# Performance work log

Hardware: AMD Instinct MI355X
Metric: run time of the kernel (lower is better)

## Reference

```python
import jax, jax.numpy as jnp
import numpy as np

B, T, E, H = 2, 4096, 768, 12
D = E // H  # head_dim = 64


def setup_inputs() -> dict:
    key = jax.random.key(0)
    ks = jax.random.split(key, 9)
    s = 1.0 / np.sqrt(E)
    return {
        "x": jax.random.normal(ks[0], (B, T, E), dtype=jnp.float32),
        "wq": jax.random.normal(ks[1], (E, E), dtype=jnp.float32) * s,
        "bq": jnp.zeros((E,), dtype=jnp.float32),
        "wk": jax.random.normal(ks[2], (E, E), dtype=jnp.float32) * s,
        "bk": jnp.zeros((E,), dtype=jnp.float32),
        "wv": jax.random.normal(ks[3], (E, E), dtype=jnp.float32) * s,
        "bv": jnp.zeros((E,), dtype=jnp.float32),
        "wo": jax.random.normal(ks[4], (E, E), dtype=jnp.float32) * s,
        "bo": jnp.zeros((E,), dtype=jnp.float32),
    }


def reference(x, wq, bq, wk, bk, wv, bv, wo, bo):
    # Linear projections (torch Linear: x @ W.T + b; weights here stored as (in,out))
    q = x @ wq + bq  # (B,T,E)
    k = x @ wk + bk
    v = x @ wv + bv

    def split(t):
        return t.reshape(B, T, H, D).transpose(0, 2, 1, 3)  # (B,H,T,D)

    q, k, v = split(q), split(k), split(v)
    scale = 1.0 / np.sqrt(D).astype(np.float32)
    scores = jnp.einsum("bhtd,bhsd->bhts", q, k) * scale  # (B,H,T,T)
    causal = jnp.tril(jnp.ones((T, T), dtype=bool))
    scores = jnp.where(causal, scores, -jnp.inf)
    attn = jax.nn.softmax(scores, axis=-1)
    out = jnp.einsum("bhts,bhsd->bhtd", attn, v)  # (B,H,T,D)
    out = out.transpose(0, 2, 1, 3).reshape(B, T, E)
    return out @ wo + bo
```

## Files before the change

### kernel.cpp

```cpp
#include <hip/hip_runtime.h>
#include <hip/hip_bf16.h>

#define TSEQ 4096
#define EMB 768
#define NH 12
#define DH 64
#define BT 8192

typedef __attribute__((ext_vector_type(8))) short bf16x8;
typedef __attribute__((ext_vector_type(4))) float f32x4;

#define FENCE() asm volatile("" ::: "memory")

__device__ __forceinline__ f32x4 mfma16(bf16x8 a, bf16x8 b, f32x4 c) {
    return __builtin_amdgcn_mfma_f32_16x16x32_bf16(a, b, c, 0, 0, 0);
}

__device__ __forceinline__ void gload16(const void* g, void* l) {
    __builtin_amdgcn_global_load_lds((const __attribute__((address_space(1))) void*)g,
                                     (__attribute__((address_space(3))) void*)l, 16, 0, 0);
}

__global__ __launch_bounds__(256) void conv_x_k(const float* __restrict__ x,
                                                __hip_bfloat16* __restrict__ xb) {
    int i = (blockIdx.x * 256 + threadIdx.x) * 4;
    float4 v = *(const float4*)(x + i);
    union { unsigned short u[4]; uint2 p; } o;
    __hip_bfloat16 t0 = __float2bfloat16(v.x); o.u[0] = *(unsigned short*)&t0;
    __hip_bfloat16 t1 = __float2bfloat16(v.y); o.u[1] = *(unsigned short*)&t1;
    __hip_bfloat16 t2 = __float2bfloat16(v.z); o.u[2] = *(unsigned short*)&t2;
    __hip_bfloat16 t3 = __float2bfloat16(v.w); o.u[3] = *(unsigned short*)&t3;
    *(uint2*)(xb + i) = o.p;
}

__global__ __launch_bounds__(256) void conv_w_k(const float* w0, const float* w1,
                                                const float* w2, const float* w3,
                                                __hip_bfloat16* o0, __hip_bfloat16* o1,
                                                __hip_bfloat16* o2, __hip_bfloat16* o3) {
    const float* w; __hip_bfloat16* o;
    switch (blockIdx.z) {
        case 0: w = w0; o = o0; break;
        case 1: w = w1; o = o1; break;
        case 2: w = w2; o = o2; break;
        default: w = w3; o = o3; break;
    }
    __shared__ float tile[32][33];
    int tx = threadIdx.x & 31, ty = threadIdx.x >> 5;
    int kb = blockIdx.y * 32, nb = blockIdx.x * 32;
    for (int i = 0; i < 32; i += 8)
        tile[ty + i][tx] = w[(size_t)(kb + ty + i) * EMB + nb + tx];
    __syncthreads();
    for (int i = 0; i < 32; i += 8)
        o[(size_t)(nb + ty + i) * EMB + kb + tx] = __float2bfloat16(tile[tx][ty + i]);
}

__device__ __forceinline__ void gemm_body(const __hip_bfloat16* __restrict__ A,
                                          const __hip_bfloat16* __restrict__ Wt,
                                          const float* __restrict__ bias,
                                          void* __restrict__ outp, int mode, float scale) {
    __shared__ alignas(16) char As[2][8192];
    __shared__ alignas(16) char Bs[2][8192];
    const int m0 = blockIdx.x * 128, n0 = blockIdx.y * 128;
    const int tid = threadIdx.x;
    const int lane = tid & 63, l15 = lane & 15, lg = lane >> 4;
    const int wave = tid >> 6, wm = wave >> 1, wn = wave & 1;
    const int swz = (l15 & 7) << 4;

    int mrow_[2]; int kelem_[2];
#pragma unroll
    for (int c = 0; c < 2; ++c) {
        int p = c * 4096 + tid * 16;
        int lrow = p >> 7, w = p & 127;
        int wp = w ^ ((lrow & 7) << 4);
        mrow_[c] = lrow + ((wp >> 6) & 1) * 64;
        kelem_[c] = (wp & 63) >> 1;
    }

    f32x4 acc[4][4];
    for (int i = 0; i < 4; ++i)
        for (int j = 0; j < 4; ++j) acc[i][j] = (f32x4){0.f, 0.f, 0.f, 0.f};

    auto stage = [&](int buf, int k0) {
#pragma unroll
        for (int c = 0; c < 2; ++c)
            gload16(A + (size_t)(m0 + mrow_[c]) * EMB + k0 + kelem_[c],
                    As[buf] + c * 4096 + wave * 1024);
#pragma unroll
        for (int c = 0; c < 2; ++c)
            gload16(Wt + (size_t)(n0 + mrow_[c]) * EMB + k0 + kelem_[c],
                    Bs[buf] + c * 4096 + wave * 1024);
    };

    stage(0, 0);
    const int NK = EMB / 32;
    for (int ks = 0; ks < NK; ++ks) {
        const int cur = ks & 1;
        const bool pre = (ks + 1 < NK);
        if (pre) stage(cur ^ 1, (ks + 1) * 32);
        if (pre) asm volatile("s_waitcnt vmcnt(4)" ::: "memory");
        else     asm volatile("s_waitcnt vmcnt(0)" ::: "memory");
        FENCE(); __builtin_amdgcn_s_barrier(); FENCE();
        bf16x8 af[4], bfv[4];
#pragma unroll
        for (int f = 0; f < 4; ++f)
            af[f] = *(const bf16x8*)(As[cur] + (f * 16 + l15) * 128 + ((wm * 64 + lg * 16) ^ swz));
#pragma unroll
        for (int f = 0; f < 4; ++f)
            bfv[f] = *(const bf16x8*)(Bs[cur] + (f * 16 + l15) * 128 + ((wn * 64 + lg * 16) ^ swz));
        __builtin_amdgcn_s_setprio(1);
#pragma unroll
        for (int i = 0; i < 4; ++i)
#pragma unroll
            for (int j = 0; j < 4; ++j)
                acc[i][j] = mfma16(af[i], bfv[j], acc[i][j]);
        __builtin_amdgcn_s_setprio(0);
        FENCE(); __builtin_amdgcn_s_barrier(); FENCE();
    }

#pragma unroll
    for (int i = 0; i < 4; ++i) {
#pragma unroll
        for (int j = 0; j < 4; ++j) {
            const int n = n0 + wn * 64 + j * 16 + l15;
            const float bv = bias[n];
            const int mbase = m0 + wm * 64 + i * 16 + lg * 4;
#pragma unroll
            for (int r = 0; r < 4; ++r) {
                const int m = mbase + r;
                const float val = (acc[i][j][r] + bv) * scale;
                if (mode == 2) {
                    ((float*)outp)[(size_t)m * EMB + n] = val;
                } else {
                    const int b = m >> 12, t = m & (TSEQ - 1);
                    const int h = n >> 6, d = n & 63;
                    size_t addr;
                    if (mode == 0) addr = ((size_t)(b * NH + h) * TSEQ + t) * DH + d;
                    else           addr = ((size_t)(b * NH + h) * DH + d) * TSEQ + t;
                    ((__hip_bfloat16*)outp)[addr] = __float2bfloat16(val);
                }
            }
        }
    }
}

__global__ __launch_bounds__(256) void qkv_k(const __hip_bfloat16* __restrict__ xb,
                                             const __hip_bfloat16* __restrict__ wqT,
                                             const __hip_bfloat16* __restrict__ wkT,
                                             const __hip_bfloat16* __restrict__ wvT,
                                             const float* __restrict__ bq,
                                             const float* __restrict__ bk,
                                             const float* __restrict__ bv,
                                             __hip_bfloat16* __restrict__ qo,
                                             __hip_bfloat16* __restrict__ ko,
                                             __hip_bfloat16* __restrict__ vo) {
    const __hip_bfloat16* Wt; const float* bias; void* o; int mode; float scale;
    const float cq = 0.125f * 1.44269504089f;
    switch (blockIdx.z) {
        case 0:  Wt = wqT; bias = bq; o = qo; mode = 0; scale = cq;  break;
        case 1:  Wt = wkT; bias = bk; o = ko; mode = 0; scale = 1.f; break;
        default: Wt = wvT; bias = bv; o = vo; mode = 1; scale = 1.f; break;
    }
    gemm_body(xb, Wt, bias, o, mode, scale);
}

__global__ __launch_bounds__(256) void oproj_k(const __hip_bfloat16* __restrict__ abf,
                                               const __hip_bfloat16* __restrict__ woT,
                                               const float* __restrict__ bo,
                                               float* __restrict__ out) {
    gemm_body(abf, woT, bo, out, 2, 1.f);
}

__global__ __launch_bounds__(256, 3) void attn_k(const __hip_bfloat16* __restrict__ qb,
                                                 const __hip_bfloat16* __restrict__ kb,
                                                 const __hip_bfloat16* __restrict__ vt,
                                                 __hip_bfloat16* __restrict__ ab) {
    __shared__ alignas(16) char Ks[2][8192];
    __shared__ alignas(16) char Vs[2][8192];
    __shared__ alignas(16) char pbuf[4][4096];
    const int lane = threadIdx.x & 63, l15 = lane & 15, lg = lane >> 4;
    const int wave = threadIdx.x >> 6;
    const int bid = blockIdx.x;
    const int xcd = bid & 7, slot = bid >> 3;
    const int pair = slot & 31, hgrp = slot >> 5;
    const int bh = xcd + hgrp * 8;
    const __hip_bfloat16* Qh = qb + (size_t)bh * TSEQ * DH;
    const __hip_bfloat16* Kh = kb + (size_t)bh * TSEQ * DH;
    const __hip_bfloat16* Vh = vt + (size_t)bh * DH * TSEQ;
    char* Pb = pbuf[wave];
    const int swz = (l15 & 7) << 4;
    const int b = bh / NH, h = bh % NH;
    const float M0 = 12.0f;

    bf16x8 ones8;
#pragma unroll
    for (int j = 0; j < 8; ++j) ones8[j] = (short)0x3F80;

    unsigned ka[8];
#pragma unroll
    for (int st = 0; st < 4; ++st)
#pragma unroll
        for (int ks = 0; ks < 2; ++ks)
            ka[st * 2 + ks] = (unsigned)((st * 16 + l15) * 128 + ((ks * 64 + lg * 16) ^ swz));
    char* pwh[4]; char* prh[2]; char* pwl[4]; char* prl[2];
#pragma unroll
    for (int st = 0; st < 4; ++st) {
        pwh[st] = Pb + l15 * 128 + ((st * 32 + lg * 8) ^ swz);
        pwl[st] = pwh[st] + 2048;
    }
#pragma unroll
    for (int ks = 0; ks < 2; ++ks) {
        prh[ks] = Pb + l15 * 128 + ((ks * 64 + lg * 16) ^ swz);
        prl[ks] = prh[ks] + 2048;
    }
    const int dthr = wave * 16 + l15 - lg * 4;

    int r_[2], wp_[2];
#pragma unroll
    for (int c = 0; c < 2; ++c) {
        int p = c * 4096 + wave * 1024 + lane * 16;
        int r = p >> 7, w = p & 127;
        r_[c] = r;
        wp_[c] = (w ^ ((r & 7) << 4)) >> 1;
    }

    const int lo = pair, hi = 63 - pair;
    const int q0l = lo * 64 + wave * 16;
    const int q0h = hi * 64 + wave * 16;
    const int nsb = hi + 1;

    bf16x8 qh0 = *(const bf16x8*)(Qh + (size_t)(q0h + l15) * DH + lg * 8);
    bf16x8 qh1 = *(const bf16x8*)(Qh + (size_t)(q0h + l15) * DH + 32 + lg * 8);
    bf16x8 ql0 = *(const bf16x8*)(Qh + (size_t)(q0l + l15) * DH + lg * 8);
    bf16x8 ql1 = *(const bf16x8*)(Qh + (size_t)(q0l + l15) * DH + 32 + lg * 8);

    f32x4 oh[4], ol[4];
#pragma unroll
    for (int dt = 0; dt < 4; ++dt) { oh[dt] = (f32x4){0.f,0.f,0.f,0.f}; ol[dt] = (f32x4){0.f,0.f,0.f,0.f}; }
    f32x4 lh = (f32x4){0.f,0.f,0.f,0.f}, ll = (f32x4){0.f,0.f,0.f,0.f};

    const char* kg0 = (const char*)(Kh + (size_t)r_[0] * DH + wp_[0]);
    const char* kg1 = (const char*)(Kh + (size_t)r_[1] * DH + wp_[1]);
    const char* vg0 = (const char*)(Vh + (size_t)r_[0] * TSEQ + wp_[0]);
    const char* vg1 = (const char*)(Vh + (size_t)r_[1] * TSEQ + wp_[1]);

#define STAGE(DST) do {                                                          \
    gload16(kg0, Ks[DST] + wave * 1024);                                         \
    gload16(kg1, Ks[DST] + 4096 + wave * 1024);                                  \
    gload16(vg0, Vs[DST] + wave * 1024);                                         \
    gload16(vg1, Vs[DST] + 4096 + wave * 1024);                                  \
    kg0 += 8192; kg1 += 8192; vg0 += 128; vg1 += 128;                            \
} while (0)

#define QKSM(KF, Q0, Q1, MASKB, PW) do {                                         \
    f32x4 sa[4];                                                                 \
    __builtin_amdgcn_s_setprio(1);                                               \
    _Pragma("unroll")                                                            \
    for (int st = 0; st < 4; ++st) {                                             \
        f32x4 z = (f32x4){0.f, 0.f, 0.f, 0.f};                                   \
        z = mfma16(KF[st * 2 + 0], Q0, z);                                       \
        z = mfma16(KF[st * 2 + 1], Q1, z);                                       \
        sa[st] = z;                                                              \
    }                                                                            \
    __builtin_amdgcn_s_setprio(0);                                               \
    if (MASKB) {                                                                 \
        _Pragma("unroll")                                                        \
        for (int st = 0; st < 4; ++st)                                           \
            _Pragma("unroll")                                                    \
            for (int r = 0; r < 4; ++r)                                          \
                if (st * 16 + r > dthr) sa[st][r] = -INFINITY;                   \
    }                                                                            \
    _Pragma("unroll")                                                            \
    for (int st = 0; st < 4; ++st) {                                             \
        const float e0 = exp2f(sa[st][0] - M0);                                  \
        const float e1 = exp2f(sa[st][1] - M0);                                  \
        const float e2 = exp2f(sa[st][2] - M0);                                  \
        const float e3 = exp2f(sa[st][3] - M0);                                  \
        uint2 pkv;                                                               \
        asm("v_cvt_pk_bf16_f32 %0, %1, %2" : "=v"(pkv.x) : "v"(e0), "v"(e1));    \
        asm("v_cvt_pk_bf16_f32 %0, %1, %2" : "=v"(pkv.y) : "v"(e2), "v"(e3));    \
        *(uint2*)PW[st] = pkv;                                                   \
    }                                                                            \
} while (0)

#define PVU(VF, OV, LA, PR) do {                                                 \
    bf16x8 pf0 = *(const bf16x8*)PR[0];                                          \
    bf16x8 pf1 = *(const bf16x8*)PR[1];                                          \
    __builtin_amdgcn_s_setprio(1);                                               \
    LA = mfma16(pf0, ones8, LA);                                                 \
    LA = mfma16(pf1, ones8, LA);                                                 \
    _Pragma("unroll")                                                            \
    for (int dt = 0; dt < 4; ++dt)                                               \
        OV[dt] = mfma16(pf0, VF[dt * 2 + 0], OV[dt]);                            \
    _Pragma("unroll")                                                            \
    for (int dt = 0; dt < 4; ++dt)                                               \
        OV[dt] = mfma16(pf1, VF[dt * 2 + 1], OV[dt]);                            \
    __builtin_amdgcn_s_setprio(0);                                               \
} while (0)

#define SBODY(BUF, PRE, LOACT, MHI, MLO) do {                                    \
    asm volatile("s_waitcnt vmcnt(0)" ::: "memory");                             \
    FENCE(); __builtin_amdgcn_s_barrier(); FENCE();                              \
    if (PRE) STAGE((BUF) ^ 1);                                                   \
    bf16x8 kf[8];                                                                \
    _Pragma("unroll")                                                            \
    for (int i = 0; i < 8; ++i) kf[i] = *(const bf16x8*)(Ks[BUF] + ka[i]);       \
    QKSM(kf, qh0, qh1, MHI, pwh);                                                \
    if (LOACT) QKSM(kf, ql0, ql1, MLO, pwl);                                     \
    bf16x8 vf[8];                                                                \
    _Pragma("unroll")                                                            \
    for (int i = 0; i < 8; ++i) vf[i] = *(const bf16x8*)(Vs[BUF] + ka[i]);       \
    asm volatile("s_waitcnt lgkmcnt(0)" ::: "memory");                           \
    PVU(vf, oh, lh, prh);                                                        \
    if (LOACT) PVU(vf, ol, ll, prl);                                             \
} while (0)

    STAGE(0);
    int sb = 0;
    while (sb + 2 <= nsb) {
        SBODY(0, true, sb <= lo, false, sb == lo);
        SBODY(1, sb + 2 < nsb, sb + 1 <= lo, sb + 1 == nsb - 1, sb + 1 == lo);
        sb += 2;
    }
    if (sb < nsb) SBODY(0, false, sb <= lo, true, sb == lo);

#undef SBODY
#undef PVU
#undef QKSM
#undef STAGE

    {
        float inv[4];
#pragma unroll
        for (int r = 0; r < 4; ++r) inv[r] = 1.0f / lh[r];
#pragma unroll
        for (int r = 0; r < 4; ++r) {
            const int qrow = q0h + lg * 4 + r;
            const size_t rowbase = ((size_t)b * TSEQ + qrow) * EMB + h * DH;
#pragma unroll
            for (int dt = 0; dt < 4; ++dt)
                ab[rowbase + dt * 16 + l15] = __float2bfloat16(oh[dt][r] * inv[r]);
        }
    }
    {
        float inv[4];
#pragma unroll
        for (int r = 0; r < 4; ++r) inv[r] = 1.0f / ll[r];
#pragma unroll
        for (int r = 0; r < 4; ++r) {
            const int qrow = q0l + lg * 4 + r;
            const size_t rowbase = ((size_t)b * TSEQ + qrow) * EMB + h * DH;
#pragma unroll
            for (int dt = 0; dt < 4; ++dt)
                ab[rowbase + dt * 16 + l15] = __float2bfloat16(ol[dt][r] * inv[r]);
        }
    }
}

extern "C" void kernel_launch(void* const* d_in, const int* in_sizes, int n_in,
                              void* d_out, int out_size, void* d_ws, size_t ws_size,
                              hipStream_t stream) {
    (void)in_sizes; (void)n_in; (void)out_size; (void)ws_size;
    const float* x  = (const float*)d_in[0];
    const float* wq = (const float*)d_in[1];
    const float* bq = (const float*)d_in[2];
    const float* wk = (const float*)d_in[3];
    const float* bk = (const float*)d_in[4];
    const float* wv = (const float*)d_in[5];
    const float* bv = (const float*)d_in[6];
    const float* wo = (const float*)d_in[7];
    const float* bo = (const float*)d_in[8];
    float* out = (float*)d_out;

    char* ws = (char*)d_ws;
    size_t off = 0;
    auto alloc = [&](size_t bytes) {
        char* p = ws + off;
        off += (bytes + 255) & ~(size_t)255;
        return p;
    };
    __hip_bfloat16* xb  = (__hip_bfloat16*)alloc((size_t)BT * EMB * 2);
    __hip_bfloat16* qbf = (__hip_bfloat16*)alloc((size_t)BT * EMB * 2);
    __hip_bfloat16* kbf = (__hip_bfloat16*)alloc((size_t)BT * EMB * 2);
    __hip_bfloat16* vtb = (__hip_bfloat16*)alloc((size_t)BT * EMB * 2);
    __hip_bfloat16* abf = (__hip_bfloat16*)alloc((size_t)BT * EMB * 2);
    __hip_bfloat16* wqT = (__hip_bfloat16*)alloc((size_t)EMB * EMB * 2);
    __hip_bfloat16* wkT = (__hip_bfloat16*)alloc((size_t)EMB * EMB * 2);
    __hip_bfloat16* wvT = (__hip_bfloat16*)alloc((size_t)EMB * EMB * 2);
    __hip_bfloat16* woT = (__hip_bfloat16*)alloc((size_t)EMB * EMB * 2);

    conv_x_k<<<BT * EMB / 1024, 256, 0, stream>>>(x, xb);
    conv_w_k<<<dim3(24, 24, 4), 256, 0, stream>>>(wq, wk, wv, wo, wqT, wkT, wvT, woT);
    qkv_k<<<dim3(64, 6, 3), 256, 0, stream>>>(xb, wqT, wkT, wvT, bq, bk, bv, qbf, kbf, vtb);
    attn_k<<<768, 256, 0, stream>>>(qbf, kbf, vtb, abf);
    oproj_k<<<dim3(64, 6), 256, 0, stream>>>(abf, woT, bo, out);
}
```

Baseline: 190.1 us.

## Use 64-row output-projection tiles and rotate attention pair order per head group

Replaces the shared gemm_body output projection with a dedicated kernel using 64x128 tiles, doubling the grid from 384 to 768 blocks so the GPU's compute units are better filled. The new kernel double-buffers LDS via global_load_lds and writes fp32 output with bias. Separately, attention block scheduling offsets the query-pair index by head group so causal-work imbalance is spread across concurrently scheduled blocks. Smaller tiles lower per-block reuse of the weight tile and raise global traffic.

```diff
diff --git a/kernel.cpp b/kernel.cpp
--- a/kernel.cpp
+++ b/kernel.cpp
@@ -163,11 +163,87 @@
     gemm_body(xb, Wt, bias, o, mode, scale);
 }
 
-__global__ __launch_bounds__(256) void oproj_k(const __hip_bfloat16* __restrict__ abf,
-                                               const __hip_bfloat16* __restrict__ woT,
-                                               const float* __restrict__ bo,
-                                               float* __restrict__ out) {
-    gemm_body(abf, woT, bo, out, 2, 1.f);
+__global__ __launch_bounds__(256) void oproj64_k(const __hip_bfloat16* __restrict__ A,
+                                                 const __hip_bfloat16* __restrict__ Wt,
+                                                 const float* __restrict__ bias,
+                                                 float* __restrict__ out) {
+    __shared__ alignas(16) char As[2][4096];
+    __shared__ alignas(16) char Bs[2][8192];
+    const int m0 = blockIdx.x * 64, n0 = blockIdx.y * 128;
+    const int tid = threadIdx.x;
+    const int lane = tid & 63, l15 = lane & 15, lg = lane >> 4;
+    const int wave = tid >> 6, wm = wave >> 1, wn = wave & 1;
+    const int swz = (l15 & 7) << 4;
+
+    int amrow, akelem;
+    {
+        int p = tid * 16;
+        int lrow = p >> 7, w = p & 127;
+        int wp = w ^ ((lrow & 7) << 4);
+        amrow = lrow + ((wp >> 6) & 1) * 32;
+        akelem = (wp & 63) >> 1;
+    }
+    int bnrow[2], bkelem[2];
+#pragma unroll
+    for (int c = 0; c < 2; ++c) {
+        int p = c * 4096 + tid * 16;
+        int lrow = p >> 7, w = p & 127;
+        int wp = w ^ ((lrow & 7) << 4);
+        bnrow[c] = lrow + ((wp >> 6) & 1) * 64;
+        bkelem[c] = (wp & 63) >> 1;
+    }
+
+    f32x4 acc[2][4];
+    for (int i = 0; i < 2; ++i)
+        for (int j = 0; j < 4; ++j) acc[i][j] = (f32x4){0.f, 0.f, 0.f, 0.f};
+
+    auto stage = [&](int buf, int k0) {
+        gload16(A + (size_t)(m0 + amrow) * EMB + k0 + akelem,
+                As[buf] + wave * 1024);
+#pragma unroll
+        for (int c = 0; c < 2; ++c)
+            gload16(Wt + (size_t)(n0 + bnrow[c]) * EMB + k0 + bkelem[c],
+                    Bs[buf] + c * 4096 + wave * 1024);
+    };
+
+    stage(0, 0);
+    const int NK = EMB / 32;
+    for (int ks = 0; ks < NK; ++ks) {
+        const int cur = ks & 1;
+        const bool pre = (ks + 1 < NK);
+        if (pre) stage(cur ^ 1, (ks + 1) * 32);
+        if (pre) asm volatile("s_waitcnt vmcnt(3)" ::: "memory");
+        else     asm volatile("s_waitcnt vmcnt(0)" ::: "memory");
+        FENCE(); __builtin_amdgcn_s_barrier(); FENCE();
+        bf16x8 af[2], bfv[4];
+#pragma unroll
+        for (int f = 0; f < 2; ++f)
+            af[f] = *(const bf16x8*)(As[cur] + (f * 16 + l15) * 128 + ((wm * 64 + lg * 16) ^ swz));
+#pragma unroll
+        for (int f = 0; f < 4; ++f)
+            bfv[f] = *(const bf16x8*)(Bs[cur] + (f * 16 + l15) * 128 + ((wn * 64 + lg * 16) ^ swz));
+        __builtin_amdgcn_s_setprio(1);
+#pragma unroll
+        for (int i = 0; i < 2; ++i)
+#pragma unroll
+            for (int j = 0; j < 4; ++j)
+                acc[i][j] = mfma16(af[i], bfv[j], acc[i][j]);
+        __builtin_amdgcn_s_setprio(0);
+        FENCE(); __builtin_amdgcn_s_barrier(); FENCE();
+    }
+
+#pragma unroll
+    for (int i = 0; i < 2; ++i) {
+#pragma unroll
+        for (int j = 0; j < 4; ++j) {
+            const int n = n0 + wn * 64 + j * 16 + l15;
+            const float bv = bias[n];
+            const int mbase = m0 + wm * 32 + i * 16 + lg * 4;
+#pragma unroll
+            for (int r = 0; r < 4; ++r)
+                out[(size_t)(mbase + r) * EMB + n] = acc[i][j][r] + bv;
+        }
+    }
 }
 
 __global__ __launch_bounds__(256, 3) void attn_k(const __hip_bfloat16* __restrict__ qb,
@@ -181,7 +257,8 @@
     const int wave = threadIdx.x >> 6;
     const int bid = blockIdx.x;
     const int xcd = bid & 7, slot = bid >> 3;
-    const int pair = slot & 31, hgrp = slot >> 5;
+    const int hgrp = slot >> 5;
+    const int pair = ((slot & 31) + hgrp * 11) & 31;
     const int bh = xcd + hgrp * 8;
     const __hip_bfloat16* Qh = qb + (size_t)bh * TSEQ * DH;
     const __hip_bfloat16* Kh = kb + (size_t)bh * TSEQ * DH;
@@ -392,5 +469,5 @@
     conv_w_k<<<dim3(24, 24, 4), 256, 0, stream>>>(wq, wk, wv, wo, wqT, wkT, wvT, woT);
     qkv_k<<<dim3(64, 6, 3), 256, 0, stream>>>(xb, wqT, wkT, wvT, bq, bk, bv, qbf, kbf, vtb);
     attn_k<<<768, 256, 0, stream>>>(qbf, kbf, vtb, abf);
-    oproj_k<<<dim3(64, 6), 256, 0, stream>>>(abf, woT, bo, out);
-}
+    oproj64_k<<<dim3(128, 6), 256, 0, stream>>>(abf, woT, bo, out);
+}
```

Result: no change. 189.7 us (-0.2%).
